# Kernel tuning notes

Measured on AMD Instinct MI355X. Metric: run time of the kernel, lower is better.

## Reference

```python
import jax, jax.numpy as jnp
import numpy as np

NUM_BINS = 32
FAIRNESS_PENALTY = 0.1
SENSITIVE = (0, 5)


def setup_inputs() -> dict:
    key = jax.random.key(0)
    k1, k2, k3, k4 = jax.random.split(key, 4)
    B, F, P = 65536, 256, 32
    x = jax.random.uniform(k1, (B, F), dtype=jnp.float32)  # features in [0,1)
    W = jax.random.normal(k2, (F, NUM_BINS), dtype=jnp.float32) * 0.1  # main-effect weights
    IW = jax.random.normal(k3, (P, NUM_BINS, NUM_BINS), dtype=jnp.float32) * 0.1  # pairwise weights
    intercept = jax.random.normal(k4, (1,), dtype=jnp.float32)
    # build(): feature_bins[i] = linspace(0, 1, num_bins+1) for every feature
    bins = jnp.tile(jnp.linspace(0.0, 1.0, NUM_BINS + 1, dtype=jnp.float32)[None, :], (F, 1))
    pair_i = jnp.arange(P, dtype=jnp.int32) * 2  # interaction_terms = [(0,1),(2,3),...]
    pair_j = pair_i + 1
    return dict(x=x, W=W, IW=IW, intercept=intercept, bins=bins, pair_i=pair_i, pair_j=pair_j)


def _bin_indices(x, bins):
    # x: [B,F], bins: [F,NB+1] -> int32 [B,F]; matches tf sum(x>=bins)-1 with clip
    idx = jnp.sum((x[:, :, None] >= bins[None, :, :]).astype(jnp.int32), axis=-1) - 1
    return jnp.clip(idx, 0, NUM_BINS - 1)


def reference(x, W, IW, intercept, bins, pair_i, pair_j):
    B, F = x.shape
    P = IW.shape[0]
    idx = _bin_indices(x, bins)  # [B,F]
    main = W[jnp.arange(F)[None, :], idx]  # per-feature gathered contributions [B,F]
    inter = IW[jnp.arange(P)[None, :], idx[:, pair_i], idx[:, pair_j]]  # [B,P]
    preds = intercept[0] + main.sum(axis=1) + inter.sum(axis=1)  # [B]
    fairness_loss = FAIRNESS_PENALTY * sum(jnp.var(main[:, s]) for s in SENSITIVE)
    return preds[:, None], fairness_loss
```

## Files before the change

kernel.cpp:

```cpp
#include <hip/hip_runtime.h>


#define F        256
#define NBINS    32
#define WPB      16
#define BLOCK    (WPB * 64)
#define GRID     256
#define WPAD     36

__global__ __launch_bounds__(BLOCK, 4) void febm_main(
    const float* __restrict__ x, const float* __restrict__ W,
    const float* __restrict__ IW, const float* __restrict__ intercept,
    float* __restrict__ out, float4* __restrict__ partials, int B)
{
    __shared__ __align__(16) float Wl[F * WPAD];
    __shared__ float4 mm[WPB];

    {
        const float4* W4 = (const float4*)W;
        #pragma unroll
        for (int i = threadIdx.x; i < (F * NBINS) / 4; i += BLOCK) {
            const int f = i >> 3, m = i & 7;
            *(float4*)&Wl[f * WPAD + 4 * m] = W4[i];
        }
    }
    __syncthreads();

    const int lane = threadIdx.x & 63;
    const int wave = threadIdx.x >> 6;
    const int g    = lane >> 4;
    const int t    = lane & 15;
    const int gw   = blockIdx.x * WPB + wave;
    const int total_waves = GRID * WPB;
    const float c0 = intercept[0];
    const float* WlB = Wl + 4 * t * WPAD;
    const float* IWa = IW + (2 * t)     * (NBINS * NBINS);
    const float* IWb = IW + (2 * t + 1) * (NBINS * NBINS);

    float s0 = 0.f, ss0 = 0.f, s5 = 0.f, ss5 = 0.f;
    const int RG = B >> 2;

    float4 xv[4];
    if (gw < RG) {
        const float4* xr = (const float4*)(x + (size_t)(gw * 4 + g) * F);
        #pragma unroll
        for (int j = 0; j < 4; ++j) xv[j] = xr[t + j * 16];
    }

    for (int rg = gw; rg < RG; rg += total_waves) {
        const int nrg = rg + total_waves;
        float4 xn[4];
        if (nrg < RG) {
            const float4* xr = (const float4*)(x + (size_t)(nrg * 4 + g) * F);
            #pragma unroll
            for (int j = 0; j < 4; ++j) xn[j] = xr[t + j * 16];
        }

        const int row = rg * 4 + g;

        const float xe0[4] = {xv[0].x, xv[0].y, xv[0].z, xv[0].w};
        int kk[4];
        float w0[4];
        #pragma unroll
        for (int i = 0; i < 4; ++i) {
            int k = (int)(xe0[i] * 32.0f);
            kk[i] = k > NBINS - 1 ? NBINS - 1 : k;
            w0[i] = WlB[i * WPAD + kk[i]];
        }
        const float ivA = IWa[kk[0] * NBINS + kk[1]];
        const float ivB = IWb[kk[2] * NBINS + kk[3]];

        float msum = (w0[0] + w0[1]) + (w0[2] + w0[3]);
        const float mA = w0[0];
        const float mB = w0[1];

        #pragma unroll
        for (int j = 1; j < 4; ++j) {
            const float xe[4] = {xv[j].x, xv[j].y, xv[j].z, xv[j].w};
            #pragma unroll
            for (int i = 0; i < 4; ++i) {
                int k = (int)(xe[i] * 32.0f);
                k = k > NBINS - 1 ? NBINS - 1 : k;
                msum += WlB[(64 * j + i) * WPAD + k];
            }
        }

        float tot = msum + ivA + ivB;
        tot += __shfl_xor(tot, 8);
        tot += __shfl_xor(tot, 4);
        tot += __shfl_xor(tot, 2);
        tot += __shfl_xor(tot, 1);

        if (t == 0) {
            out[row] = c0 + tot;
            s0 += mA; ss0 += mA * mA;
        } else if (t == 1) {
            s5 += mB; ss5 += mB * mB;
        }

        #pragma unroll
        for (int j = 0; j < 4; ++j) xv[j] = xn[j];
    }

    float4 acc = make_float4(s0, ss0, s5, ss5);
    #pragma unroll
    for (int off = 32; off > 0; off >>= 1) {
        acc.x += __shfl_xor(acc.x, off);
        acc.y += __shfl_xor(acc.y, off);
        acc.z += __shfl_xor(acc.z, off);
        acc.w += __shfl_xor(acc.w, off);
    }
    if (lane == 0) mm[wave] = acc;
    __syncthreads();

    if (threadIdx.x == 0) {
        float4 a = mm[0];
        #pragma unroll
        for (int w = 1; w < WPB; ++w) {
            a.x += mm[w].x; a.y += mm[w].y; a.z += mm[w].z; a.w += mm[w].w;
        }
        partials[blockIdx.x] = a;
    }
}

__global__ __launch_bounds__(256) void febm_reduce(
    const float4* __restrict__ partials, int nPart, float* __restrict__ fair_out, int B)
{
    __shared__ float4 sw[4];
    const int lane = threadIdx.x & 63;
    const int wave = threadIdx.x >> 6;

    float4 a = make_float4(0.f, 0.f, 0.f, 0.f);
    for (int i = threadIdx.x; i < nPart; i += 256) {
        const float4 p = partials[i];
        a.x += p.x; a.y += p.y; a.z += p.z; a.w += p.w;
    }
    #pragma unroll
    for (int off = 32; off > 0; off >>= 1) {
        a.x += __shfl_xor(a.x, off);
        a.y += __shfl_xor(a.y, off);
        a.z += __shfl_xor(a.z, off);
        a.w += __shfl_xor(a.w, off);
    }
    if (lane == 0) sw[wave] = a;
    __syncthreads();
    if (threadIdx.x == 0) {
        float4 tt = sw[0];
        #pragma unroll
        for (int w = 1; w < 4; ++w) {
            tt.x += sw[w].x; tt.y += sw[w].y; tt.z += sw[w].z; tt.w += sw[w].w;
        }
        const double invB = 1.0 / (double)B;
        const double mean0 = tt.x * invB, mean5 = tt.z * invB;
        const double var0 = tt.y * invB - mean0 * mean0;
        const double var5 = tt.w * invB - mean5 * mean5;
        fair_out[0] = (float)(0.1 * (var0 + var5));
    }
}

extern "C" void kernel_launch(void* const* d_in, const int* in_sizes, int n_in,
                              void* d_out, int out_size, void* d_ws, size_t ws_size,
                              hipStream_t stream)
{
    const float* x         = (const float*)d_in[0];
    const float* W         = (const float*)d_in[1];
    const float* IW        = (const float*)d_in[2];
    const float* intercept = (const float*)d_in[3];

    float* out = (float*)d_out;
    const int B = in_sizes[0] / F;
    float4* partials = (float4*)d_ws;

    febm_main<<<GRID, BLOCK, 0, stream>>>(x, W, IW, intercept, out, partials, B);
    febm_reduce<<<1, 256, 0, stream>>>(partials, GRID, out + B, B);
}
```

Measured before the change: 109.0 us.

## Issue all row loads upfront and overlap W staging with x fetch

Replaces the software-pipelined grid-stride loop with a fixed unrolled set of TRIPS=4 row groups per wave, issuing all x loads and the W loads before the shared-memory store and barrier. This lets the global-memory latency for x overlap the W table staging and raises memory-level parallelism. It also drops the bin clamp to 31 and the occupancy hint in launch_bounds. The cost is higher register pressure. Rows beyond GRID*WPB*TRIPS*4 are silently skipped, and inputs equal to 1.0 would index out of range.

```diff
diff --git a/kernel.cpp b/kernel.cpp
--- a/kernel.cpp
+++ b/kernel.cpp
@@ -6,9 +6,10 @@
 #define WPB      16
 #define BLOCK    (WPB * 64)
 #define GRID     256
+#define TRIPS    4
 #define WPAD     36
 
-__global__ __launch_bounds__(BLOCK, 4) void febm_main(
+__global__ __launch_bounds__(BLOCK) void febm_main(
     const float* __restrict__ x, const float* __restrict__ W,
     const float* __restrict__ IW, const float* __restrict__ intercept,
     float* __restrict__ out, float4* __restrict__ partials, int B)
@@ -16,90 +17,96 @@
     __shared__ __align__(16) float Wl[F * WPAD];
     __shared__ float4 mm[WPB];
 
-    {
-        const float4* W4 = (const float4*)W;
-        #pragma unroll
-        for (int i = threadIdx.x; i < (F * NBINS) / 4; i += BLOCK) {
-            const int f = i >> 3, m = i & 7;
-            *(float4*)&Wl[f * WPAD + 4 * m] = W4[i];
-        }
-    }
-    __syncthreads();
-
     const int lane = threadIdx.x & 63;
     const int wave = threadIdx.x >> 6;
     const int g    = lane >> 4;
     const int t    = lane & 15;
     const int gw   = blockIdx.x * WPB + wave;
     const int total_waves = GRID * WPB;
+    const int RG = B >> 2;
+
+    const float4* W4 = (const float4*)W;
+    float4 wr0 = W4[threadIdx.x];
+    float4 wr1 = W4[threadIdx.x + BLOCK];
+
+    float4 xv[TRIPS][4];
+    #pragma unroll
+    for (int p = 0; p < TRIPS; ++p) {
+        const int rg = gw + p * total_waves;
+        if (rg < RG) {
+            const float4* xr = (const float4*)(x + (size_t)(rg * 4 + g) * F);
+            #pragma unroll
+            for (int j = 0; j < 4; ++j) xv[p][j] = xr[t + j * 16];
+        }
+    }
+
+    {
+        const int i0 = threadIdx.x;
+        const int i1 = threadIdx.x + BLOCK;
+        *(float4*)&Wl[(i0 >> 3) * WPAD + 4 * (i0 & 7)] = wr0;
+        *(float4*)&Wl[(i1 >> 3) * WPAD + 4 * (i1 & 7)] = wr1;
+    }
+    __syncthreads();
+
     const float c0 = intercept[0];
     const float* WlB = Wl + 4 * t * WPAD;
     const float* IWa = IW + (2 * t)     * (NBINS * NBINS);
     const float* IWb = IW + (2 * t + 1) * (NBINS * NBINS);
 
-    float s0 = 0.f, ss0 = 0.f, s5 = 0.f, ss5 = 0.f;
-    const int RG = B >> 2;
-
-    float4 xv[4];
-    if (gw < RG) {
-        const float4* xr = (const float4*)(x + (size_t)(gw * 4 + g) * F);
-        #pragma unroll
-        for (int j = 0; j < 4; ++j) xv[j] = xr[t + j * 16];
+    float msum[TRIPS], ivA[TRIPS], ivB[TRIPS], mA[TRIPS], mB[TRIPS];
+    #pragma unroll
+    for (int p = 0; p < TRIPS; ++p) {
+        if (gw + p * total_waves < RG) {
+            const float xe0[4] = {xv[p][0].x, xv[p][0].y, xv[p][0].z, xv[p][0].w};
+            int kk[4];
+            float w0[4];
+            #pragma unroll
+            for (int i = 0; i < 4; ++i) {
+                kk[i] = (int)(xe0[i] * 32.0f);
+                w0[i] = WlB[i * WPAD + kk[i]];
+            }
+            ivA[p] = IWa[kk[0] * NBINS + kk[1]];
+            ivB[p] = IWb[kk[2] * NBINS + kk[3]];
+            msum[p] = (w0[0] + w0[1]) + (w0[2] + w0[3]);
+            mA[p] = w0[0];
+            mB[p] = w0[1];
+        } else {
+            msum[p] = ivA[p] = ivB[p] = mA[p] = mB[p] = 0.f;
+        }
     }
 
-    for (int rg = gw; rg < RG; rg += total_waves) {
-        const int nrg = rg + total_waves;
-        float4 xn[4];
-        if (nrg < RG) {
-            const float4* xr = (const float4*)(x + (size_t)(nrg * 4 + g) * F);
-            #pragma unroll
-            for (int j = 0; j < 4; ++j) xn[j] = xr[t + j * 16];
-        }
-
-        const int row = rg * 4 + g;
-
-        const float xe0[4] = {xv[0].x, xv[0].y, xv[0].z, xv[0].w};
-        int kk[4];
-        float w0[4];
+    #pragma unroll
+    for (int j = 1; j < 4; ++j) {
         #pragma unroll
-        for (int i = 0; i < 4; ++i) {
-            int k = (int)(xe0[i] * 32.0f);
-            kk[i] = k > NBINS - 1 ? NBINS - 1 : k;
-            w0[i] = WlB[i * WPAD + kk[i]];
-        }
-        const float ivA = IWa[kk[0] * NBINS + kk[1]];
-        const float ivB = IWb[kk[2] * NBINS + kk[3]];
-
-        float msum = (w0[0] + w0[1]) + (w0[2] + w0[3]);
-        const float mA = w0[0];
-        const float mB = w0[1];
-
-        #pragma unroll
-        for (int j = 1; j < 4; ++j) {
-            const float xe[4] = {xv[j].x, xv[j].y, xv[j].z, xv[j].w};
-            #pragma unroll
-            for (int i = 0; i < 4; ++i) {
-                int k = (int)(xe[i] * 32.0f);
-                k = k > NBINS - 1 ? NBINS - 1 : k;
-                msum += WlB[(64 * j + i) * WPAD + k];
+        for (int p = 0; p < TRIPS; ++p) {
+            if (gw + p * total_waves < RG) {
+                const float xe[4] = {xv[p][j].x, xv[p][j].y, xv[p][j].z, xv[p][j].w};
+                float s = 0.f;
+                #pragma unroll
+                for (int i = 0; i < 4; ++i)
+                    s += WlB[(64 * j + i) * WPAD + (int)(xe[i] * 32.0f)];
+                msum[p] += s;
             }
         }
+    }
 
-        float tot = msum + ivA + ivB;
-        tot += __shfl_xor(tot, 8);
-        tot += __shfl_xor(tot, 4);
-        tot += __shfl_xor(tot, 2);
-        tot += __shfl_xor(tot, 1);
-
-        if (t == 0) {
-            out[row] = c0 + tot;
-            s0 += mA; ss0 += mA * mA;
-        } else if (t == 1) {
-            s5 += mB; ss5 += mB * mB;
+    float s0 = 0.f, ss0 = 0.f, s5 = 0.f, ss5 = 0.f;
+    #pragma unroll
+    for (int p = 0; p < TRIPS; ++p) {
+        const int rg = gw + p * total_waves;
+        if (rg < RG) {
+            float tot = msum[p] + ivA[p] + ivB[p];
+            tot += __shfl_xor(tot, 8);
+            tot += __shfl_xor(tot, 4);
+            tot += __shfl_xor(tot, 2);
+            tot += __shfl_xor(tot, 1);
+            if (t == 0) {
+                out[rg * 4 + g] = c0 + tot;
+                s0 += mA[p]; ss0 += mA[p] * mA[p];
+            } else if (t == 1) {
+                s5 += mB[p]; ss5 += mB[p] * mB[p];
+            }
         }
-
-        #pragma unroll
-        for (int j = 0; j < 4; ++j) xv[j] = xn[j];
     }
 
     float4 acc = make_float4(s0, ss0, s5, ss5);
```

Measured after the change: 112.2 us. 2.9% more time.
